# Optimization experiments

Measured on AMD Instinct MI355X. Metric: run time of the kernel, lower is better.

## Reference

```python
import jax, jax.numpy as jnp
import numpy as np
import math

DIM = 1024
H = 16
D = 64
M = 64  # num_features
B = 1
N = 2048


def _orf_omega(key):
    # Orthogonal Random Features: stack Q^T blocks from QR of Gaussian [D,D]
    blocks = []
    n_blocks = (M + D - 1) // D
    for i in range(n_blocks):
        G = jax.random.normal(jax.random.fold_in(key, i), (D, D), dtype=jnp.float32)
        Q, _ = jnp.linalg.qr(G)
        blocks.append(Q.T)
    return jnp.concatenate(blocks, axis=0)[:M]  # [M, D]


def setup_inputs() -> dict:
    key = jax.random.key(0)
    ks = jax.random.split(key, 7)
    inner = H * D
    x = jax.random.normal(ks[0], (B, N, DIM), dtype=jnp.float32)
    omega = _orf_omega(ks[1])
    wq = jax.random.normal(ks[2], (inner, DIM), dtype=jnp.float32) * 0.02
    wk = jax.random.normal(ks[3], (inner, DIM), dtype=jnp.float32) * 0.02
    wv = jax.random.normal(ks[4], (inner, DIM), dtype=jnp.float32) * 0.02
    wo = jax.random.normal(ks[5], (DIM, inner), dtype=jnp.float32) * 0.02
    bo = jnp.zeros((DIM,), dtype=jnp.float32)
    return {"x": x, "omega": omega, "wq": wq, "wk": wk, "wv": wv, "wo": wo, "bo": bo}


def _phi(x, omega):
    # x: [B,H,N,D], omega: [M,D] -> [B,H,N,M]
    proj = jnp.einsum('bhnd,md->bhnm', x, omega)
    norm = 0.5 * jnp.sum(x * x, axis=-1, keepdims=True)
    return jnp.exp(proj - norm) / math.sqrt(M)


def _heads(t):
    b, n, _ = t.shape
    return t.reshape(b, n, H, D).transpose(0, 2, 1, 3)  # [B,H,N,D]


def reference(x, omega, wq, wk, wv, wo, bo):
    b, n, _ = x.shape
    q = _heads(x @ wq.T)
    k = _heads(x @ wk.T)
    v = _heads(x @ wv.T)
    phi_q = _phi(q, omega)  # [B,H,N,M]
    phi_k = _phi(k, omega)
    # causal linear attention: cumulative KV state (naive materialization, faithful to source)
    kv = jnp.einsum('bhnm,bhnd->bhnmd', phi_k, v)       # [B,H,N,M,D]
    kv_cumsum = jnp.cumsum(kv, axis=2)
    k_cumsum = jnp.cumsum(phi_k, axis=2)                # [B,H,N,M]
    out = jnp.einsum('bhnm,bhnmd->bhnd', phi_q, kv_cumsum)
    z = 1.0 / (jnp.einsum('bhnm,bhnm->bhn', phi_q, k_cumsum) + 1e-6)
    out = out * z[..., None]
    out = out.transpose(0, 2, 1, 3).reshape(b, n, H * D)
    return out @ wo.T + bo
```

## Files before the change

kernel.cpp:

```cpp
#include <hip/hip_runtime.h>
#include <hip/hip_bf16.h>

typedef __hip_bfloat16 bf16;
typedef __attribute__((ext_vector_type(8))) short bf16x8;
typedef __attribute__((ext_vector_type(8))) _Float16 f16x8;
typedef __attribute__((ext_vector_type(4))) float f32x4;

constexpr int N_TOK = 2048;
constexpr int DIMM  = 1024;
constexpr int NH    = 16;
constexpr int HD    = 64;
constexpr int FM    = 64;
constexpr int NC    = 32;
constexpr int CS    = 64;

__device__ __forceinline__ float b2f(bf16 v) { return __bfloat162float(v); }
__device__ __forceinline__ unsigned short f2bfu(float v) {
  bf16 h = __float2bfloat16(v);
  return *reinterpret_cast<unsigned short*>(&h);
}
__device__ __forceinline__ unsigned short f2hu(float v) {
  _Float16 h = (_Float16)v;
  return *reinterpret_cast<unsigned short*>(&h);
}

__device__ __forceinline__ void gl_lds16(const void* g, short* l) {
  __builtin_amdgcn_global_load_lds(
      (const __attribute__((address_space(1))) void*)g,
      (__attribute__((address_space(3))) void*)l, 16, 0, 0);
}

__device__ __forceinline__ void split_pack_bf(const float4 v, uint2& ph, uint2& pl) {
  float f[4] = {v.x, v.y, v.z, v.w};
  unsigned short h[4], l[4];
  #pragma unroll
  for (int j = 0; j < 4; j++) {
    bf16 hb = __float2bfloat16(f[j]);
    h[j] = *reinterpret_cast<unsigned short*>(&hb);
    l[j] = f2bfu(f[j] - b2f(hb));
  }
  ph.x = (unsigned)h[0] | ((unsigned)h[1] << 16);
  ph.y = (unsigned)h[2] | ((unsigned)h[3] << 16);
  pl.x = (unsigned)l[0] | ((unsigned)l[1] << 16);
  pl.y = (unsigned)l[2] | ((unsigned)l[3] << 16);
}

__global__ __launch_bounds__(256) void cvt_all(
    const float4* __restrict__ x, const float4* __restrict__ wq,
    const float4* __restrict__ wk, const float4* __restrict__ wv,
    const float4* __restrict__ wo,
    _Float16* __restrict__ x16, _Float16* __restrict__ w16,
    bf16* __restrict__ wo_bf)
{
  int i = blockIdx.x * 256 + threadIdx.x;
  if (i < 524288) {
    float4 v = x[i];
    uint2 p = { (unsigned)f2hu(v.x) | ((unsigned)f2hu(v.y) << 16),
                (unsigned)f2hu(v.z) | ((unsigned)f2hu(v.w) << 16) };
    reinterpret_cast<uint2*>(x16)[i] = p;
  } else if (i < 1310720) {
    int j = i - 524288;
    const float4* src = (j < 262144) ? wq : (j < 524288) ? wk : wv;
    int jj = (j < 262144) ? j : (j < 524288) ? j - 262144 : j - 524288;
    float4 v = src[jj];
    uint2 p = { (unsigned)f2hu(v.x) | ((unsigned)f2hu(v.y) << 16),
                (unsigned)f2hu(v.z) | ((unsigned)f2hu(v.w) << 16) };
    reinterpret_cast<uint2*>(w16)[j] = p;
  } else {
    int j = i - 1310720;
    float4 v = wo[j];
    uint2 p = { (unsigned)f2bfu(v.x) | ((unsigned)f2bfu(v.y) << 16),
                (unsigned)f2bfu(v.z) | ((unsigned)f2bfu(v.w) << 16) };
    reinterpret_cast<uint2*>(wo_bf)[j] = p;
  }
}

__global__ __launch_bounds__(512, 4) void gemm_qkv_phi(
    const _Float16* __restrict__ A16, const _Float16* __restrict__ B16,
    const float* __restrict__ omega,
    bf16* __restrict__ phiq, bf16* __restrict__ phik, bf16* __restrict__ Cv)
{
  constexpr int K = 1024;
  __shared__ alignas(16) char smemRaw[32768];
  short* sA = (short*)smemRaw;
  short* sB = sA + 8192;

  const int tid = threadIdx.x, lane = tid & 63, wv = tid >> 6;
  const int colBase = blockIdx.x * 128, rowBase = blockIdx.y * 128;
  const int waveRow = (wv >> 2) * 64, waveCol = (wv & 3) * 32;
  const int stR = tid >> 2, stK = (tid & 3) * 8;

  const _Float16* gA = A16 + (size_t)(rowBase + stR) * K + stK;
  const _Float16* gB = B16 + (size_t)(colBase + stR) * K + stK;
  const int ldsOff = wv * 512;

  f32x4 acc[4][2];
  #pragma unroll
  for (int r = 0; r < 4; r++)
    #pragma unroll
    for (int c = 0; c < 2; c++) acc[r][c] = (f32x4){0.f, 0.f, 0.f, 0.f};

  const int frow = lane & 15, fk = (lane >> 4) * 8, quad = lane >> 4;
  const int nIter = K / 32;

  gl_lds16(gA, &sA[ldsOff]);
  gl_lds16(gB, &sB[ldsOff]);

  int buf = 0;
  for (int it = 0; it < nIter; it++) {
    __syncthreads();
    if (it + 1 < nIter) {
      const size_t kb = (size_t)(it + 1) * 32;
      const int nb = buf ^ 1;
      gl_lds16(gA + kb, &sA[nb * 4096 + ldsOff]);
      gl_lds16(gB + kb, &sB[nb * 4096 + ldsOff]);
    }
    f16x8 a[4], b[2];
    #pragma unroll
    for (int r = 0; r < 4; r++)
      a[r] = *reinterpret_cast<const f16x8*>(&sA[buf * 4096 + (waveRow + r * 16 + frow) * 32 + fk]);
    #pragma unroll
    for (int c = 0; c < 2; c++)
      b[c] = *reinterpret_cast<const f16x8*>(&sB[buf * 4096 + (waveCol + c * 16 + frow) * 32 + fk]);
    #pragma unroll
    for (int r = 0; r < 4; r++)
      #pragma unroll
      for (int c = 0; c < 2; c++)
        acc[r][c] = __builtin_amdgcn_mfma_f32_16x16x32_f16(a[r], b[c], acc[r][c], 0, 0, 0);
    buf ^= 1;
  }
  __syncthreads();

  if (colBase >= 2048) {
    #pragma unroll
    for (int r = 0; r < 4; r++)
      #pragma unroll
      for (int c = 0; c < 2; c++)
        #pragma unroll
        for (int reg = 0; reg < 4; reg++) {
          int row = rowBase + waveRow + r * 16 + quad * 4 + reg;
          int col = colBase - 2048 + waveCol + c * 16 + (lane & 15);
          Cv[(size_t)row * 1024 + col] = __float2bfloat16(acc[r][c][reg]);
        }
    return;
  }

  constexpr int LD = 72;
  short* sQ16 = (short*)smemRaw;
  short* sO16 = sQ16 + 9216;
  float* sNorm = (float*)(sO16 + 4608);

  const bool isQ = (colBase < 1024);
  const int hPairBase = (isQ ? colBase : (colBase - 1024)) >> 6;
  bf16* dstBase = isQ ? phiq : phik;
  const int headSel = (wv & 3) >> 1;

  {
    int r = tid >> 3, cg = (tid & 7) * 8;
    const float* src = omega + r * 64 + cg;
    float4 v0 = *reinterpret_cast<const float4*>(src);
    float4 v1 = *reinterpret_cast<const float4*>(src + 4);
    uint4 p = { (unsigned)f2hu(v0.x) | ((unsigned)f2hu(v0.y) << 16),
                (unsigned)f2hu(v0.z) | ((unsigned)f2hu(v0.w) << 16),
                (unsigned)f2hu(v1.x) | ((unsigned)f2hu(v1.y) << 16),
                (unsigned)f2hu(v1.z) | ((unsigned)f2hu(v1.w) << 16) };
    *reinterpret_cast<uint4*>(&sO16[r * LD + cg]) = p;
  }
  if (tid < 256) sNorm[tid] = 0.f;
  __syncthreads();

  #pragma unroll
  for (int r = 0; r < 4; r++)
    #pragma unroll
    for (int reg = 0; reg < 4; reg++) {
      float s = acc[r][0][reg] * acc[r][0][reg] + acc[r][1][reg] * acc[r][1][reg];
      s += __shfl_xor(s, 1); s += __shfl_xor(s, 2);
      s += __shfl_xor(s, 4); s += __shfl_xor(s, 8);
      if ((lane & 15) == 0) {
        int row = waveRow + r * 16 + quad * 4 + reg;
        atomicAdd(&sNorm[headSel * 128 + row], s);
      }
    }

  #pragma unroll
  for (int hh = 0; hh < 2; hh++) {
    if (headSel == hh) {
      #pragma unroll
      for (int r = 0; r < 4; r++)
        #pragma unroll
        for (int c = 0; c < 2; c++)
          #pragma unroll
          for (int reg = 0; reg < 4; reg++) {
            int row = waveRow + r * 16 + quad * 4 + reg;
            int lc = (waveCol & 63) + c * 16 + (lane & 15);
            sQ16[row * LD + lc] = (short)f2hu(acc[r][c][reg]);
          }
    }
    __syncthreads();

    f32x4 acc2[4];
    #pragma unroll
    for (int ct = 0; ct < 4; ct++) acc2[ct] = (f32x4){0.f, 0.f, 0.f, 0.f};
    #pragma unroll
    for (int ks = 0; ks < 64; ks += 32) {
      f16x8 a = *reinterpret_cast<const f16x8*>(&sQ16[(wv * 16 + frow) * LD + ks + fk]);
      #pragma unroll
      for (int ct = 0; ct < 4; ct++) {
        f16x8 b = *reinterpret_cast<const f16x8*>(&sO16[(ct * 16 + frow) * LD + ks + fk]);
        acc2[ct] = __builtin_amdgcn_mfma_f32_16x16x32_f16(a, b, acc2[ct], 0, 0, 0);
      }
    }
    const int h = hPairBase + hh;
    #pragma unroll
    for (int ct = 0; ct < 4; ct++)
      #pragma unroll
      for (int reg = 0; reg < 4; reg++) {
        int row = wv * 16 + quad * 4 + reg;
        int m = ct * 16 + (lane & 15);
        float norm = 0.5f * sNorm[hh * 128 + row];
        float v = __expf(fminf(acc2[ct][reg] - norm, 80.f)) * 0.125f;
        dstBase[((size_t)h * N_TOK + rowBase + row) * FM + m] = __float2bfloat16(v);
      }
    __syncthreads();
  }
}

__global__ __launch_bounds__(512) void gemm_bf16_out(
    const bf16* __restrict__ A, const bf16* __restrict__ B,
    const float* __restrict__ bias, float* __restrict__ C)
{
  constexpr int K = 1024;
  __shared__ short sA[2][2048], sB[2][4096];
  const int tid = threadIdx.x, lane = tid & 63, wv = tid >> 6;
  const int rowBase = blockIdx.y * 64, colBase = blockIdx.x * 128;
  const int waveRow = (wv >> 2) * 32, waveCol = (wv & 3) * 32;
  const int stR = tid >> 2, stK = (tid & 3) * 8;
  const bf16* gA = A + (size_t)(rowBase + stR) * K + stK;
  const bf16* gB = B + (size_t)(colBase + stR) * K + stK;
  const int ldsOff = wv * 512;

  f32x4 acc[2][2];
  #pragma unroll
  for (int r = 0; r < 2; r++)
    #pragma unroll
    for (int c = 0; c < 2; c++) acc[r][c] = (f32x4){0.f, 0.f, 0.f, 0.f};

  const int frow = lane & 15, fk = (lane >> 4) * 8;
  const int nIter = K / 32;

  if (wv < 4) gl_lds16(gA, &sA[0][ldsOff]);
  gl_lds16(gB, &sB[0][ldsOff]);

  int buf = 0;
  for (int it = 0; it < nIter; it++) {
    __syncthreads();
    if (it + 1 < nIter) {
      const size_t kb = (size_t)(it + 1) * 32;
      const int nb = buf ^ 1;
      if (wv < 4) gl_lds16(gA + kb, &sA[nb][ldsOff]);
      gl_lds16(gB + kb, &sB[nb][ldsOff]);
    }
    bf16x8 a[2], b[2];
    #pragma unroll
    for (int r = 0; r < 2; r++)
      a[r] = *reinterpret_cast<const bf16x8*>(&sA[buf][(waveRow + r * 16 + frow) * 32 + fk]);
    #pragma unroll
    for (int c = 0; c < 2; c++)
      b[c] = *reinterpret_cast<const bf16x8*>(&sB[buf][(waveCol + c * 16 + frow) * 32 + fk]);
    #pragma unroll
    for (int r = 0; r < 2; r++)
      #pragma unroll
      for (int c = 0; c < 2; c++)
        acc[r][c] = __builtin_amdgcn_mfma_f32_16x16x32_bf16(a[r], b[c], acc[r][c], 0, 0, 0);
    buf ^= 1;
  }

  #pragma unroll
  for (int r = 0; r < 2; r++)
    #pragma unroll
    for (int c = 0; c < 2; c++)
      #pragma unroll
      for (int reg = 0; reg < 4; reg++) {
        int row = rowBase + waveRow + r * 16 + (lane >> 4) * 4 + reg;
        int col = colBase + waveCol + c * 16 + (lane & 15);
        C[(size_t)row * 1024 + col] = acc[r][c][reg] + bias[col];
      }
}

__global__ __launch_bounds__(256) void chunk_sum(
    const bf16* __restrict__ phik, const bf16* __restrict__ vf,
    float* __restrict__ ckv_t, float* __restrict__ ck)
{
  constexpr int LD = 72;
  __shared__ short sVt[64 * LD], sPkt[64 * LD];
  __shared__ float sCp[64][4];
  const int c = blockIdx.x, h = blockIdx.y;
  const int tid = threadIdx.x, lane = tid & 63, wv = tid >> 6;

  {
    int j = tid >> 2, g = tid & 3;
    const bf16* vs = vf + (size_t)(c * CS + j) * DIMM + h * HD + g * 16;
    uint4 v0 = *reinterpret_cast<const uint4*>(vs);
    uint4 v1 = *reinterpret_cast<const uint4*>(vs + 8);
    const unsigned short* pv = (const unsigned short*)&v0;
    #pragma unroll
    for (int e = 0; e < 8; e++) sVt[(g * 16 + e) * LD + j] = (short)pv[e];
    pv = (const unsigned short*)&v1;
    #pragma unroll
    for (int e = 0; e < 8; e++) sVt[(g * 16 + 8 + e) * LD + j] = (short)pv[e];

    const bf16* ks = phik + ((size_t)h * N_TOK + c * CS + j) * FM + g * 16;
    uint4 k0 = *reinterpret_cast<const uint4*>(ks);
    uint4 k1 = *reinterpret_cast<const uint4*>(ks + 8);
    pv = (const unsigned short*)&k0;
    #pragma unroll
    for (int e = 0; e < 8; e++) sPkt[(g * 16 + e) * LD + j] = (short)pv[e];
    pv = (const unsigned short*)&k1;
    #pragma unroll
    for (int e = 0; e < 8; e++) sPkt[(g * 16 + 8 + e) * LD + j] = (short)pv[e];
  }
  __syncthreads();

  const int frow = lane & 15, fk = (lane >> 4) * 8;
  const int rowW = wv * 16;

  f32x4 acc[4];
  #pragma unroll
  for (int mt = 0; mt < 4; mt++) acc[mt] = (f32x4){0.f, 0.f, 0.f, 0.f};
  #pragma unroll
  for (int ks = 0; ks < 64; ks += 32) {
    bf16x8 a = *reinterpret_cast<const bf16x8*>(&sVt[(rowW + frow) * LD + ks + fk]);
    #pragma unroll
    for (int mt = 0; mt < 4; mt++) {
      bf16x8 b = *reinterpret_cast<const bf16x8*>(&sPkt[(mt * 16 + frow) * LD + ks + fk]);
      acc[mt] = __builtin_amdgcn_mfma_f32_16x16x32_bf16(a, b, acc[mt], 0, 0, 0);
    }
  }

  {
    int m = tid >> 2, q = tid & 3;
    float s = 0.f;
    #pragma unroll
    for (int e = 0; e < 16; e++)
      s += b2f(*reinterpret_cast<bf16*>(&sPkt[m * LD + q * 16 + e]));
    sCp[m][q] = s;
  }
  __syncthreads();
  if (tid < 64)
    ck[((size_t)h * NC + c) * FM + tid] = sCp[tid][0] + sCp[tid][1] + sCp[tid][2] + sCp[tid][3];

  float* dst = ckv_t + ((size_t)h * NC + c) * 4096;
  #pragma unroll
  for (int mt = 0; mt < 4; mt++)
    #pragma unroll
    for (int reg = 0; reg < 4; reg++) {
      int gd = rowW + (lane >> 4) * 4 + reg;
      int gm = mt * 16 + (lane & 15);
      dst[gd * 64 + gm] = acc[mt][reg];
    }
}

__global__ __launch_bounds__(256) void prefix_chunks(
    float* __restrict__ ckv, float* __restrict__ ck)
{
  const int h = blockIdx.x, g = blockIdx.y;
  const int cell = g * 256 + threadIdx.x;
  const size_t base = (size_t)h * NC * 4096 + cell;
  float v[NC];
  #pragma unroll
  for (int c = 0; c < NC; c++) v[c] = ckv[base + (size_t)c * 4096];
  float run = 0.f;
  #pragma unroll
  for (int c = 0; c < NC; c++) { float t = v[c]; ckv[base + (size_t)c * 4096] = run; run += t; }
  if (g == 0 && threadIdx.x < 64) {
    const size_t b2 = (size_t)h * NC * FM + threadIdx.x;
    float u[NC];
    #pragma unroll
    for (int c = 0; c < NC; c++) u[c] = ck[b2 + (size_t)c * FM];
    float r2 = 0.f;
    #pragma unroll
    for (int c = 0; c < NC; c++) { float t = u[c]; ck[b2 + (size_t)c * FM] = r2; r2 += t; }
  }
}

__global__ __launch_bounds__(256) void attn_chunk(
    const bf16* __restrict__ phiq, const bf16* __restrict__ phik,
    const bf16* __restrict__ vf, const float* __restrict__ ckv_t,
    const float* __restrict__ ck, bf16* __restrict__ attn_out)
{
  constexpr int LD = 72;
  __shared__ short sPq[64 * LD];
  __shared__ short sPk[64 * LD];
  __shared__ short sAl[64 * LD];
  __shared__ short sVt[64 * LD];
  __shared__ short sSh[64 * LD];
  __shared__ short sSl[64 * LD];
  __shared__ float sKc[64];
  __shared__ float sDp[64][4];
  __shared__ float sDen[64];

  const int c = blockIdx.x, h = blockIdx.y;
  const int tid = threadIdx.x, lane = tid & 63, wv = tid >> 6;

  {
    int r = tid >> 2, g = tid & 3;
    const size_t gb = ((size_t)h * N_TOK + c * CS + r) * FM + g * 16;
    uint4 q0 = *reinterpret_cast<const uint4*>(phiq + gb);
    uint4 q1 = *reinterpret_cast<const uint4*>(phiq + gb + 8);
    uint4 k0 = *reinterpret_cast<const uint4*>(phik + gb);
    uint4 k1 = *reinterpret_cast<const uint4*>(phik + gb + 8);
    int o = r * LD + g * 16;
    *reinterpret_cast<uint4*>(&sPq[o]) = q0; *reinterpret_cast<uint4*>(&sPq[o + 8]) = q1;
    *reinterpret_cast<uint4*>(&sPk[o]) = k0; *reinterpret_cast<uint4*>(&sPk[o + 8]) = k1;
  }
  {
    int j = tid >> 2, g = tid & 3;
    const bf16* vs = vf + (size_t)(c * CS + j) * DIMM + h * HD + g * 16;
    uint4 v0 = *reinterpret_cast<const uint4*>(vs);
    uint4 v1 = *reinterpret_cast<const uint4*>(vs + 8);
    const unsigned short* pv = (const unsigned short*)&v0;
    #pragma unroll
    for (int e = 0; e < 8; e++) sVt[(g * 16 + e) * LD + j] = (short)pv[e];
    pv = (const unsigned short*)&v1;
    #pragma unroll
    for (int e = 0; e < 8; e++) sVt[(g * 16 + 8 + e) * LD + j] = (short)pv[e];
  }
  {
    int d = tid >> 2, mg = tid & 3;
    const float* src = ckv_t + ((size_t)h * NC + c) * 4096 + d * 64 + mg * 16;
    int o = d * LD + mg * 16;
    #pragma unroll
    for (int e4 = 0; e4 < 4; e4++) {
      float4 v = *reinterpret_cast<const float4*>(src + e4 * 4);
      uint2 ph, pl;
      split_pack_bf(v, ph, pl);
      *reinterpret_cast<uint2*>(&sSh[o + e4 * 4]) = ph;
      *reinterpret_cast<uint2*>(&sSl[o + e4 * 4]) = pl;
    }
  }
  if (tid < 64) sKc[tid] = ck[((size_t)h * NC + c) * FM + tid];
  __syncthreads();

  const int frow = lane & 15, fk = (lane >> 4) * 8;
  const int rowW = wv * 16;

  f32x4 accA[4];
  #pragma unroll
  for (int ct = 0; ct < 4; ct++) accA[ct] = (f32x4){0.f, 0.f, 0.f, 0.f};
  #pragma unroll
  for (int ks = 0; ks < 64; ks += 32) {
    bf16x8 a = *reinterpret_cast<const bf16x8*>(&sPq[(rowW + frow) * LD + ks + fk]);
    #pragma unroll
    for (int ct = 0; ct < 4; ct++) {
      bf16x8 b = *reinterpret_cast<const bf16x8*>(&sPk[(ct * 16 + frow) * LD + ks + fk]);
      accA[ct] = __builtin_amdgcn_mfma_f32_16x16x32_bf16(a, b, accA[ct], 0, 0, 0);
    }
  }
  __syncthreads();

  #pragma unroll
  for (int ct = 0; ct < 4; ct++)
    #pragma unroll
    for (int reg = 0; reg < 4; reg++) {
      int gi = rowW + (lane >> 4) * 4 + reg;
      int gj = ct * 16 + (lane & 15);
      float av = (gj <= gi) ? accA[ct][reg] : 0.f;
      bf16 hb = __float2bfloat16(av);
      sPk[gi * LD + gj] = *reinterpret_cast<short*>(&hb);
      unsigned short lu = f2bfu(av - b2f(hb));
      sAl[gi * LD + gj] = (short)lu;
    }
  __syncthreads();

  {
    int i = tid >> 2, q = tid & 3;
    float p = 0.f;
    #pragma unroll
    for (int e = 0; e < 16; e++) {
      int m = q * 16 + e;
      p += b2f(*reinterpret_cast<bf16*>(&sPq[i * LD + m])) * sKc[m];
      p += b2f(*reinterpret_cast<bf16*>(&sPk[i * LD + m]))
         + b2f(*reinterpret_cast<bf16*>(&sAl[i * LD + m]));
    }
    sDp[i][q] = p;
  }

  f32x4 accO[4];
  #pragma unroll
  for (int dt = 0; dt < 4; dt++) accO[dt] = (f32x4){0.f, 0.f, 0.f, 0.f};
  #pragma unroll
  for (int ks = 0; ks < 64; ks += 32) {
    bf16x8 ah = *reinterpret_cast<const bf16x8*>(&sPk[(rowW + frow) * LD + ks + fk]);
    bf16x8 al = *reinterpret_cast<const bf16x8*>(&sAl[(rowW + frow) * LD + ks + fk]);
    bf16x8 aq = *reinterpret_cast<const bf16x8*>(&sPq[(rowW + frow) * LD + ks + fk]);
    #pragma unroll
    for (int dt = 0; dt < 4; dt++) {
      bf16x8 bv = *reinterpret_cast<const bf16x8*>(&sVt[(dt * 16 + frow) * LD + ks + fk]);
      bf16x8 bh = *reinterpret_cast<const bf16x8*>(&sSh[(dt * 16 + frow) * LD + ks + fk]);
      bf16x8 bl = *reinterpret_cast<const bf16x8*>(&sSl[(dt * 16 + frow) * LD + ks + fk]);
      accO[dt] = __builtin_amdgcn_mfma_f32_16x16x32_bf16(ah, bv, accO[dt], 0, 0, 0);
      accO[dt] = __builtin_amdgcn_mfma_f32_16x16x32_bf16(al, bv, accO[dt], 0, 0, 0);
      accO[dt] = __builtin_amdgcn_mfma_f32_16x16x32_bf16(aq, bh, accO[dt], 0, 0, 0);
      accO[dt] = __builtin_amdgcn_mfma_f32_16x16x32_bf16(aq, bl, accO[dt], 0, 0, 0);
    }
  }
  __syncthreads();
  if (tid < 64) {
    float den = sDp[tid][0] + sDp[tid][1] + sDp[tid][2] + sDp[tid][3];
    sDen[tid] = 1.f / (den + 1e-6f);
  }
  __syncthreads();

  #pragma unroll
  for (int dt = 0; dt < 4; dt++)
    #pragma unroll
    for (int reg = 0; reg < 4; reg++) {
      int gi = rowW + (lane >> 4) * 4 + reg;
      int gd = dt * 16 + (lane & 15);
      float v = accO[dt][reg] * sDen[gi];
      attn_out[(size_t)(c * CS + gi) * DIMM + h * HD + gd] = __float2bfloat16(v);
    }
}

extern "C" void kernel_launch(void* const* d_in, const int* in_sizes, int n_in,
                              void* d_out, int out_size, void* d_ws, size_t ws_size,
                              hipStream_t stream) {
  (void)in_sizes; (void)n_in; (void)out_size; (void)ws_size;
  const float* x     = (const float*)d_in[0];
  const float* omega = (const float*)d_in[1];
  const float* wq    = (const float*)d_in[2];
  const float* wk    = (const float*)d_in[3];
  const float* wv    = (const float*)d_in[4];
  const float* wo    = (const float*)d_in[5];
  const float* bo    = (const float*)d_in[6];
  float* out = (float*)d_out;

  char* w = (char*)d_ws;
  _Float16* x16   = (_Float16*)(w);
  _Float16* w16   = (_Float16*)(w + (4u  << 20));
  bf16*     wo_bf = (bf16*)   (w + (10u << 20));
  bf16*     vbf   = (bf16*)   (w + (12u << 20));
  bf16*     phiq  = (bf16*)   (w + (16u << 20));
  bf16*     phik  = (bf16*)   (w + (20u << 20));
  float*    ckv   = (float*)  (w + (24u << 20));
  float*    ck    = (float*)  (w + (32u << 20));
  bf16*     attnb = (bf16*)x16;

  cvt_all<<<6144, 256, 0, stream>>>((const float4*)x, (const float4*)wq,
                                    (const float4*)wk, (const float4*)wv,
                                    (const float4*)wo,
                                    x16, w16, wo_bf);

  gemm_qkv_phi<<<dim3(24, 16), 512, 0, stream>>>(x16, w16, omega, phiq, phik, vbf);

  chunk_sum<<<dim3(NC, NH), 256, 0, stream>>>(phik, vbf, ckv, ck);
  prefix_chunks<<<dim3(NH, 16), 256, 0, stream>>>(ckv, ck);
  attn_chunk<<<dim3(NC, NH), 256, 0, stream>>>(phiq, phik, vbf, ckv, ck, attnb);

  gemm_bf16_out<<<dim3(8, 32), 512, 0, stream>>>(attnb, wo_bf, bo, out);
}
```

Before: 140.4 us.

## Use split-K waves, 64-wide K tiles and XOR-swizzled LDS in the QKV GEMM

```diff
diff --git a/kernel.cpp b/kernel.cpp
--- a/kernel.cpp
+++ b/kernel.cpp
@@ -81,67 +81,102 @@
     bf16* __restrict__ phiq, bf16* __restrict__ phik, bf16* __restrict__ Cv)
 {
   constexpr int K = 1024;
-  __shared__ alignas(16) char smemRaw[32768];
+  __shared__ alignas(16) char smemRaw[65536];
   short* sA = (short*)smemRaw;
-  short* sB = sA + 8192;
+  short* sB = sA + 16384;
 
   const int tid = threadIdx.x, lane = tid & 63, wv = tid >> 6;
   const int colBase = blockIdx.x * 128, rowBase = blockIdx.y * 128;
-  const int waveRow = (wv >> 2) * 64, waveCol = (wv & 3) * 32;
-  const int stR = tid >> 2, stK = (tid & 3) * 8;
-
-  const _Float16* gA = A16 + (size_t)(rowBase + stR) * K + stK;
-  const _Float16* gB = B16 + (size_t)(colBase + stR) * K + stK;
-  const int ldsOff = wv * 512;
-
-  f32x4 acc[4][2];
+  const int p = wv >> 1, ksub = wv & 1;
+  const int waveRow = (p >> 1) * 64, waveCol = (p & 1) * 64;
+
+  const int sRow = tid >> 3;
+  const int sCol = ((tid & 7) ^ (sRow & 7)) * 8;
+  const _Float16* gA0 = A16 + (size_t)(rowBase + sRow) * K + sCol;
+  const _Float16* gA1 = gA0 + (size_t)64 * K;
+  const _Float16* gB0 = B16 + (size_t)(colBase + sRow) * K + sCol;
+  const _Float16* gB1 = gB0 + (size_t)64 * K;
+  short* ldsA0 = sA + tid * 8;
+  short* ldsA1 = sA + tid * 8 + 4096;
+  short* ldsB0 = sB + tid * 8;
+  short* ldsB1 = sB + tid * 8 + 4096;
+
+  f32x4 acc[4][4];
   #pragma unroll
   for (int r = 0; r < 4; r++)
     #pragma unroll
-    for (int c = 0; c < 2; c++) acc[r][c] = (f32x4){0.f, 0.f, 0.f, 0.f};
-
-  const int frow = lane & 15, fk = (lane >> 4) * 8, quad = lane >> 4;
-  const int nIter = K / 32;
-
-  gl_lds16(gA, &sA[ldsOff]);
-  gl_lds16(gB, &sB[ldsOff]);
+    for (int c = 0; c < 4; c++) acc[r][c] = (f32x4){0.f, 0.f, 0.f, 0.f};
+
+  const int frow = lane & 15, quad = lane >> 4, fk = quad * 8;
+  const int xorOff = (((ksub << 2) + quad) ^ (frow & 7)) * 8;
+  const int nIter = K / 64;
+
+  gl_lds16(gA0, ldsA0); gl_lds16(gA1, ldsA1);
+  gl_lds16(gB0, ldsB0); gl_lds16(gB1, ldsB1);
 
   int buf = 0;
   for (int it = 0; it < nIter; it++) {
     __syncthreads();
     if (it + 1 < nIter) {
-      const size_t kb = (size_t)(it + 1) * 32;
-      const int nb = buf ^ 1;
-      gl_lds16(gA + kb, &sA[nb * 4096 + ldsOff]);
-      gl_lds16(gB + kb, &sB[nb * 4096 + ldsOff]);
-    }
-    f16x8 a[4], b[2];
+      const size_t kb = (size_t)(it + 1) * 64;
+      const int nb = (buf ^ 1) * 8192;
+      gl_lds16(gA0 + kb, ldsA0 + nb); gl_lds16(gA1 + kb, ldsA1 + nb);
+      gl_lds16(gB0 + kb, ldsB0 + nb); gl_lds16(gB1 + kb, ldsB1 + nb);
+    }
+    const int bo = buf * 8192;
+    f16x8 a[4], b[4];
     #pragma unroll
     for (int r = 0; r < 4; r++)
-      a[r] = *reinterpret_cast<const f16x8*>(&sA[buf * 4096 + (waveRow + r * 16 + frow) * 32 + fk]);
-    #pragma unroll
-    for (int c = 0; c < 2; c++)
-      b[c] = *reinterpret_cast<const f16x8*>(&sB[buf * 4096 + (waveCol + c * 16 + frow) * 32 + fk]);
+      a[r] = *reinterpret_cast<const f16x8*>(&sA[bo + (waveRow + r * 16 + frow) * 64 + xorOff]);
+    #pragma unroll
+    for (int c = 0; c < 4; c++)
+      b[c] = *reinterpret_cast<const f16x8*>(&sB[bo + (waveCol + c * 16 + frow) * 64 + xorOff]);
     #pragma unroll
     for (int r = 0; r < 4; r++)
       #pragma unroll
-      for (int c = 0; c < 2; c++)
+      for (int c = 0; c < 4; c++)
         acc[r][c] = __builtin_amdgcn_mfma_f32_16x16x32_f16(a[r], b[c], acc[r][c], 0, 0, 0);
     buf ^= 1;
   }
+
+  __syncthreads();
+  float* sAcc = (float*)smemRaw;
+  if (ksub) {
+    float* dstS = sAcc + p * 4096;
+    #pragma unroll
+    for (int r = 0; r < 4; r++)
+      #pragma unroll
+      for (int c = 0; c < 4; c++)
+        #pragma unroll
+        for (int reg = 0; reg < 4; reg++)
+          dstS[(r * 16 + quad * 4 + reg) * 64 + c * 16 + frow] = acc[r][c][reg];
+  }
+  __syncthreads();
+  if (!ksub) {
+    const float* srcS = sAcc + p * 4096;
+    #pragma unroll
+    for (int r = 0; r < 4; r++)
+      #pragma unroll
+      for (int c = 0; c < 4; c++)
+        #pragma unroll
+        for (int reg = 0; reg < 4; reg++)
+          acc[r][c][reg] += srcS[(r * 16 + quad * 4 + reg) * 64 + c * 16 + frow];
+  }
   __syncthreads();
 
   if (colBase >= 2048) {
-    #pragma unroll
-    for (int r = 0; r < 4; r++)
-      #pragma unroll
-      for (int c = 0; c < 2; c++)
+    if (!ksub) {
+      #pragma unroll
+      for (int r = 0; r < 4; r++)
         #pragma unroll
-        for (int reg = 0; reg < 4; reg++) {
-          int row = rowBase + waveRow + r * 16 + quad * 4 + reg;
-          int col = colBase - 2048 + waveCol + c * 16 + (lane & 15);
-          Cv[(size_t)row * 1024 + col] = __float2bfloat16(acc[r][c][reg]);
-        }
+        for (int c = 0; c < 4; c++)
+          #pragma unroll
+          for (int reg = 0; reg < 4; reg++) {
+            int row = rowBase + waveRow + r * 16 + quad * 4 + reg;
+            int col = colBase - 2048 + waveCol + c * 16 + frow;
+            Cv[(size_t)row * 1024 + col] = __float2bfloat16(acc[r][c][reg]);
+          }
+    }
     return;
   }
 
@@ -153,46 +188,47 @@
   const bool isQ = (colBase < 1024);
   const int hPairBase = (isQ ? colBase : (colBase - 1024)) >> 6;
   bf16* dstBase = isQ ? phiq : phik;
-  const int headSel = (wv & 3) >> 1;
+  const int headOwn = p & 1;
+  const bool owner = (ksub == 0);
 
   {
     int r = tid >> 3, cg = (tid & 7) * 8;
     const float* src = omega + r * 64 + cg;
     float4 v0 = *reinterpret_cast<const float4*>(src);
     float4 v1 = *reinterpret_cast<const float4*>(src + 4);
-    uint4 p = { (unsigned)f2hu(v0.x) | ((unsigned)f2hu(v0.y) << 16),
-                (unsigned)f2hu(v0.z) | ((unsigned)f2hu(v0.w) << 16),
-                (unsigned)f2hu(v1.x) | ((unsigned)f2hu(v1.y) << 16),
-                (unsigned)f2hu(v1.z) | ((unsigned)f2hu(v1.w) << 16) };
-    *reinterpret_cast<uint4*>(&sO16[r * LD + cg]) = p;
-  }
-  if (tid < 256) sNorm[tid] = 0.f;
-  __syncthreads();
-
-  #pragma unroll
-  for (int r = 0; r < 4; r++)
-    #pragma unroll
-    for (int reg = 0; reg < 4; reg++) {
-      float s = acc[r][0][reg] * acc[r][0][reg] + acc[r][1][reg] * acc[r][1][reg];
-      s += __shfl_xor(s, 1); s += __shfl_xor(s, 2);
-      s += __shfl_xor(s, 4); s += __shfl_xor(s, 8);
-      if ((lane & 15) == 0) {
-        int row = waveRow + r * 16 + quad * 4 + reg;
-        atomicAdd(&sNorm[headSel * 128 + row], s);
+    uint4 pk = { (unsigned)f2hu(v0.x) | ((unsigned)f2hu(v0.y) << 16),
+                 (unsigned)f2hu(v0.z) | ((unsigned)f2hu(v0.w) << 16),
+                 (unsigned)f2hu(v1.x) | ((unsigned)f2hu(v1.y) << 16),
+                 (unsigned)f2hu(v1.z) | ((unsigned)f2hu(v1.w) << 16) };
+    *reinterpret_cast<uint4*>(&sO16[r * LD + cg]) = pk;
+  }
+
+  if (owner) {
+    #pragma unroll
+    for (int r = 0; r < 4; r++)
+      #pragma unroll
+      for (int reg = 0; reg < 4; reg++) {
+        float s = 0.f;
+        #pragma unroll
+        for (int c = 0; c < 4; c++) s += acc[r][c][reg] * acc[r][c][reg];
+        s += __shfl_xor(s, 1); s += __shfl_xor(s, 2);
+        s += __shfl_xor(s, 4); s += __shfl_xor(s, 8);
+        if (frow == 0)
+          sNorm[headOwn * 128 + waveRow + r * 16 + quad * 4 + reg] = s;
       }
-    }
+  }
 
   #pragma unroll
   for (int hh = 0; hh < 2; hh++) {
-    if (headSel == hh) {
+    if (owner && headOwn == hh) {
       #pragma unroll
       for (int r = 0; r < 4; r++)
         #pragma unroll
-        for (int c = 0; c < 2; c++)
+        for (int c = 0; c < 4; c++)
           #pragma unroll
           for (int reg = 0; reg < 4; reg++) {
             int row = waveRow + r * 16 + quad * 4 + reg;
-            int lc = (waveCol & 63) + c * 16 + (lane & 15);
+            int lc = c * 16 + frow;
             sQ16[row * LD + lc] = (short)f2hu(acc[r][c][reg]);
           }
     }
@@ -216,7 +252,7 @@
       #pragma unroll
       for (int reg = 0; reg < 4; reg++) {
         int row = wv * 16 + quad * 4 + reg;
-        int m = ct * 16 + (lane & 15);
+        int m = ct * 16 + frow;
         float norm = 0.5f * sNorm[hh * 128 + row];
         float v = __expf(fminf(acc2[ct][reg] - norm, 80.f)) * 0.125f;
         dstBase[((size_t)h * N_TOK + rowBase + row) * FM + m] = __float2bfloat16(v);
```

Measured after the change: 177.1 us. 1.26x slower.
